# Kernel optimization log

Measured on AMD Instinct MI355X. Metric: run time of the kernel, lower is better.

The kernel has to match this reference:

```python
import jax, jax.numpy as jnp
import numpy as np

NUM_HEADS, NUM_KEYS, NUM_VALUES, NUM_OUTPUTS = 8, 64, 64, 512
B, H, W, C = 16, 64, 64, 512


def setup_inputs() -> dict:
    key = jax.random.key(0)
    ks = jax.random.split(key, 5)
    def xavier(k, shape):
        fan_in, fan_out = shape
        lim = np.sqrt(6.0 / (fan_in + fan_out))
        return jax.random.uniform(k, shape, jnp.float32, -lim, lim)
    return {
        "x": jax.random.normal(ks[0], (B, H, W, C), jnp.float32),
        "Wq": xavier(ks[1], (C, NUM_HEADS * NUM_KEYS)),
        "bq": jnp.zeros((NUM_HEADS * NUM_KEYS,), jnp.float32),
        "Wk": xavier(ks[2], (C, NUM_HEADS * NUM_KEYS)),
        "bk": jnp.zeros((NUM_HEADS * NUM_KEYS,), jnp.float32),
        "Wv": xavier(ks[3], (C, NUM_HEADS * NUM_VALUES)),
        "bv": jnp.zeros((NUM_HEADS * NUM_VALUES,), jnp.float32),
        "Wo": xavier(ks[4], (NUM_VALUES, NUM_OUTPUTS)),
        "bo": jnp.zeros((NUM_OUTPUTS,), jnp.float32),
    }


def reference(x, Wq, bq, Wk, bk, Wv, bv, Wo, bo):
    b, h, w, c = x.shape
    n, dk, dv = NUM_HEADS, NUM_KEYS, NUM_VALUES
    # single pooled query per image
    q = (jnp.mean(x, axis=(1, 2)) @ Wq + bq).reshape(b, n, dk)      # [B,N,dk]
    K = (x @ Wk + bk).reshape(b, h, w, n, dk)                        # [B,H,W,N,dk]
    V = (x @ Wv + bv).reshape(b, h, w, n, dv)                        # [B,H,W,N,dv]
    scale = 1.0 / jnp.sqrt(jnp.float32(dk))
    # scores of the single query against every pixel
    s = jnp.einsum('bnk,bhwnk->bnhw', q, K) * scale                  # [B,N,H,W]
    attn_h = jax.nn.softmax(s, axis=-1)   # per row, softmax over width
    attn_v = jax.nn.softmax(s, axis=-2)   # per column, softmax over height
    A_h = jnp.einsum('bnhw,bhwnv->bnhv', attn_h, V)                  # [B,N,H,dv]
    A_v = jnp.einsum('bnhw,bhwnv->bnwv', attn_v, V)                  # [B,N,W,dv]
    # outer-product combine over spatial dims, summed over heads
    A = jnp.einsum('bnhv,bnwv->bhwv', A_h, A_v)                      # [B,H,W,dv]
    return A @ Wo + bo                                               # [B,H,W,num_outputs]
```

## Files before the change

kernel.cpp:

```cpp
#include <hip/hip_runtime.h>
#include <hip/hip_bf16.h>

#define NHEADS 8
#define DK 64
#define DV 64
#define CIN 512
#define PIX_PER_IMG 4096
#define NPIX 65536

typedef short bf16x8 __attribute__((ext_vector_type(8)));
typedef float f32x4 __attribute__((ext_vector_type(4)));

__device__ __forceinline__ float b2f(unsigned int u) {
  union { unsigned int i; float f; } v; v.i = u << 16; return v.f;
}
__device__ __forceinline__ unsigned short f2b(float f) {
  union { float f; unsigned int i; } v; v.f = f;
  unsigned int x = v.i;
  return (unsigned short)((x + 0x7fffu + ((x >> 16) & 1u)) >> 16);
}
__device__ __forceinline__ void gload_lds16(const void* g, void* l) {
  __builtin_amdgcn_global_load_lds(
      (const __attribute__((address_space(1))) void*)g,
      (__attribute__((address_space(3))) void*)l, 16, 0, 0);
}

__global__ __launch_bounds__(256) void k_pool_prep(
    const float* __restrict__ x, unsigned short* __restrict__ xb,
    float* __restrict__ partial,
    const float* __restrict__ Wv, const float* __restrict__ Wo,
    unsigned short* __restrict__ WvT, unsigned short* __restrict__ WoT) {
  int blk = blockIdx.x;
  int t = threadIdx.x;
  if (blk >= 2048) {
    int idx = (blk - 2048) * 256 + t;
    if (idx < 262144) {
      int n = idx >> 9, c = idx & 511;
      WvT[idx] = f2b(Wv[(size_t)c * 512 + n]);
    } else {
      int j = idx - 262144;
      int o = j >> 6, kk = j & 63;
      WoT[j] = f2b(Wo[(size_t)kk * 512 + o]);
    }
    return;
  }
  __shared__ float4 sh[128];
  int b = blk >> 7, chunk = blk & 127;
  int c4 = t & 127;
  int half = t >> 7;
  size_t rowbase = (size_t)b * PIX_PER_IMG + chunk * 32;
  const float4* x4 = (const float4*)x;
  float4 acc = make_float4(0.f, 0.f, 0.f, 0.f);
#pragma unroll
  for (int i = 0; i < 16; ++i) {
    int p = 2 * i + half;
    float4 v = x4[(rowbase + p) * 128 + c4];
    acc.x += v.x; acc.y += v.y; acc.z += v.z; acc.w += v.w;
    uint2 o;
    o.x = (unsigned)f2b(v.x) | ((unsigned)f2b(v.y) << 16);
    o.y = (unsigned)f2b(v.z) | ((unsigned)f2b(v.w) << 16);
    *(uint2*)(xb + (rowbase + p) * CIN + c4 * 4) = o;
  }
  if (half) sh[c4] = acc;
  __syncthreads();
  if (!half) {
    float4 o = sh[c4];
    acc.x += o.x; acc.y += o.y; acc.z += o.z; acc.w += o.w;
    *(float4*)(partial + (size_t)blk * CIN + c4 * 4) = acc;
  }
}

__global__ __launch_bounds__(256) void k_qp2(
    const float* __restrict__ partial,
    const float* __restrict__ Wq, const float* __restrict__ bq,
    const float* __restrict__ Wk, float* __restrict__ P) {
  __shared__ float xs[CIN];
  __shared__ float red[256];
  __shared__ float qsh[64];
  int b = blockIdx.x, n = blockIdx.y, t = threadIdx.x;
  for (int c = t; c < CIN; c += 256) {
    float s = 0.f;
    for (int ch = 0; ch < 128; ++ch) s += partial[((size_t)(b * 128 + ch)) * CIN + c];
    xs[c] = s * (1.0f / 4096.0f);
  }
  __syncthreads();
  int jj = t & 63, part = t >> 6;
  {
    float acc = 0.f;
    const float* wp = Wq + (size_t)(part * 128) * CIN + n * 64 + jj;
    for (int ci = 0; ci < 128; ++ci)
      acc += xs[part * 128 + ci] * wp[(size_t)ci * CIN];
    red[t] = acc;
  }
  __syncthreads();
  if (t < 64)
    qsh[t] = red[t] + red[t + 64] + red[t + 128] + red[t + 192] + bq[n * 64 + t];
  __syncthreads();
  for (int c = t; c < CIN; c += 256) {
    float acc = 0.f;
    const float* wr = Wk + (size_t)c * CIN + n * 64;
    for (int k = 0; k < 64; ++k) acc += qsh[k] * wr[k];
    P[((size_t)(b * NHEADS + n)) * CIN + c] = acc * 0.125f;
  }
}

__global__ __launch_bounds__(256) void k_scores(
    const unsigned short* __restrict__ xb, const float* __restrict__ P,
    float* __restrict__ s) {
  __shared__ __align__(16) unsigned short Pl[24 * 520];
  int blk = blockIdx.x;
  int b = blk >> 6, tile = blk & 63;
  int t = threadIdx.x;
  for (int i = t; i < 4096; i += 256) {
    int n = i >> 9, c = i & 511;
    float pv = P[((size_t)(b * NHEADS + n)) * CIN + c];
    unsigned short h = f2b(pv);
    Pl[n * 520 + c] = h;
    Pl[(n + 8) * 520 + c] = f2b(pv - b2f(h));
  }
  __syncthreads();
  int wave = t >> 6, lane = t & 63;
  int prow = lane & 15, kgrp = lane >> 4;
  const unsigned short* arow =
      xb + ((size_t)b * PIX_PER_IMG + tile * 64 + wave * 16 + prow) * CIN + kgrp * 8;
  const unsigned short* bhi = Pl + prow * 520 + kgrp * 8;
  const unsigned short* blo = Pl + (prow + 8) * 520 + kgrp * 8;
  f32x4 acc = (f32x4){0.f, 0.f, 0.f, 0.f};
#pragma unroll
  for (int kb = 0; kb < 16; ++kb) {
    bf16x8 af = *(const bf16x8*)(arow + kb * 32);
    bf16x8 bh = *(const bf16x8*)(bhi + kb * 32);
    bf16x8 bl = *(const bf16x8*)(blo + kb * 32);
    acc = __builtin_amdgcn_mfma_f32_16x16x32_bf16(af, bh, acc, 0, 0, 0);
    acc = __builtin_amdgcn_mfma_f32_16x16x32_bf16(af, bl, acc, 0, 0, 0);
  }
  int n = prow;
  if (n < 8) {
    float* sp = s + ((size_t)(b * NHEADS + n)) * PIX_PER_IMG + tile * 64 + wave * 16 + kgrp * 4;
#pragma unroll
    for (int r = 0; r < 4; ++r) sp[r] = acc[r];
  }
}

__global__ __launch_bounds__(256) void k_xhv(
    const unsigned short* __restrict__ xb, const float* __restrict__ s,
    unsigned short* __restrict__ XHV) {
  __shared__ unsigned short xs[64 * 256];
  __shared__ float al[NHEADS * 64];
  int bx = blockIdx.x, ch = blockIdx.y, t = threadIdx.x;
  bool isV = bx >= 1024;
  int bi = isV ? bx - 1024 : bx;
  int b = bi >> 6, rc = bi & 63;
  if (!isV) {
    const unsigned short* src = xb + ((size_t)(b * PIX_PER_IMG + rc * 64)) * CIN + ch * 256;
#pragma unroll
    for (int i = 0; i < 8; ++i) {
      int idx = i * 256 + t;
      int w = idx >> 5, off = idx & 31;
      ((uint4*)xs)[idx] = ((const uint4*)(src + (size_t)w * CIN))[off];
    }
  } else {
#pragma unroll
    for (int i = 0; i < 8; ++i) {
      int idx = i * 256 + t;
      int h = idx >> 5, off = idx & 31;
      ((uint4*)xs)[idx] =
          ((const uint4*)(xb + ((size_t)(b * PIX_PER_IMG + h * 64 + rc)) * CIN + ch * 256))[off];
    }
  }
  {
    int n = t >> 5, l = t & 31;
    const float* sp = s + ((size_t)(b * NHEADS + n)) * PIX_PER_IMG;
    float v0, v1;
    if (!isV) { v0 = sp[rc * 64 + 2 * l];  v1 = sp[rc * 64 + 2 * l + 1]; }
    else      { v0 = sp[(2 * l) * 64 + rc]; v1 = sp[(2 * l + 1) * 64 + rc]; }
    float m = fmaxf(v0, v1);
#pragma unroll
    for (int mask = 1; mask <= 16; mask <<= 1) m = fmaxf(m, __shfl_xor(m, mask));
    float e0 = __expf(v0 - m), e1 = __expf(v1 - m);
    float sm = e0 + e1;
#pragma unroll
    for (int mask = 1; mask <= 16; mask <<= 1) sm += __shfl_xor(sm, mask);
    float inv = 1.f / sm;
    al[n * 64 + 2 * l] = e0 * inv;
    al[n * 64 + 2 * l + 1] = e1 * inv;
  }
  __syncthreads();
  int n = t >> 5, oct = t & 31;
  float acc[8] = {0.f, 0.f, 0.f, 0.f, 0.f, 0.f, 0.f, 0.f};
  const float* ar = al + n * 64;
  for (int p = 0; p < 64; ++p) {
    float aw = ar[p];
    uint4 u = *(const uint4*)(xs + (size_t)p * 256 + oct * 8);
    acc[0] += aw * b2f(u.x & 0xffff);
    acc[1] += aw * b2f(u.x >> 16);
    acc[2] += aw * b2f(u.y & 0xffff);
    acc[3] += aw * b2f(u.y >> 16);
    acc[4] += aw * b2f(u.z & 0xffff);
    acc[5] += aw * b2f(u.z >> 16);
    acc[6] += aw * b2f(u.w & 0xffff);
    acc[7] += aw * b2f(u.w >> 16);
  }
  uint4 o;
  o.x = (unsigned)f2b(acc[0]) | ((unsigned)f2b(acc[1]) << 16);
  o.y = (unsigned)f2b(acc[2]) | ((unsigned)f2b(acc[3]) << 16);
  o.z = (unsigned)f2b(acc[4]) | ((unsigned)f2b(acc[5]) << 16);
  o.w = (unsigned)f2b(acc[6]) | ((unsigned)f2b(acc[7]) << 16);
  size_t dst = ((size_t)(n * 2048 + (isV ? 1024 : 0) + b * 64 + rc)) * CIN + ch * 256 + oct * 8;
  *(uint4*)(XHV + dst) = o;
}

__global__ __launch_bounds__(256) void k_gemm2(
    const unsigned short* __restrict__ XHV, const unsigned short* __restrict__ WvT,
    const float* __restrict__ bv, float* __restrict__ Ah, float* __restrict__ Av) {
  __shared__ __align__(16) unsigned short As[64 * 64];
  __shared__ __align__(16) unsigned short Bs[64 * 64];
  const int t = threadIdx.x;
  const int wave = t >> 6, lane = t & 63;
  const int m0 = blockIdx.x * 64, head = blockIdx.y;
  const unsigned short* A = XHV + (size_t)head * 2048 * CIN;
  const unsigned short* BT = WvT + (size_t)head * 64 * CIN;

  f32x4 acc[4];
  for (int j = 0; j < 4; ++j) acc[j] = (f32x4){0.f, 0.f, 0.f, 0.f};

  const int lrow = wave * 8 + (lane >> 3);
  const int lcolb = (lane & 7) * 16;

  for (int kt = 0; kt < 8; ++kt) {
    __syncthreads();
#pragma unroll
    for (int j = 0; j < 2; ++j)
      gload_lds16((const char*)A + ((size_t)(m0 + j * 32 + lrow) * CIN + kt * 64) * 2 + lcolb,
                  (char*)As + (j * 32 + wave * 8) * 128);
#pragma unroll
    for (int j = 0; j < 2; ++j)
      gload_lds16((const char*)BT + ((size_t)(j * 32 + lrow) * CIN + kt * 64) * 2 + lcolb,
                  (char*)Bs + (j * 32 + wave * 8) * 128);
    __syncthreads();
#pragma unroll
    for (int ss = 0; ss < 2; ++ss) {
      bf16x8 af = *(const bf16x8*)((const char*)As + (wave * 16 + (lane & 15)) * 128 +
                                   ss * 64 + ((lane >> 4) * 16));
      bf16x8 bg[4];
#pragma unroll
      for (int j = 0; j < 4; ++j)
        bg[j] = *(const bf16x8*)((const char*)Bs + (j * 16 + (lane & 15)) * 128 +
                                 ss * 64 + ((lane >> 4) * 16));
#pragma unroll
      for (int j = 0; j < 4; ++j)
        acc[j] = __builtin_amdgcn_mfma_f32_16x16x32_bf16(af, bg[j], acc[j], 0, 0, 0);
    }
  }
#pragma unroll
  for (int j = 0; j < 4; ++j) {
    int v = j * 16 + (lane & 15);
    float bb = bv[head * 64 + v];
#pragma unroll
    for (int r = 0; r < 4; ++r) {
      int m = m0 + wave * 16 + ((lane >> 4) * 4) + r;
      float val = acc[j][r] + bb;
      if (m < 1024) {
        int b = m >> 6, h = m & 63;
        Ah[((size_t)(b * NHEADS + head)) * 4096 + h * 64 + v] = val;
      } else {
        int m2 = m - 1024;
        int b = m2 >> 6, w = m2 & 63;
        Av[((size_t)(b * NHEADS + head)) * 4096 + w * 64 + v] = val;
      }
    }
  }
}

__global__ __launch_bounds__(256) void k_outgemm(
    const float* __restrict__ Ah, const float* __restrict__ Av,
    const unsigned short* __restrict__ WoT,
    const float* __restrict__ bo, float* __restrict__ out) {
  __shared__ __align__(16) unsigned short As[128 * 64];
  __shared__ __align__(16) unsigned short Bs[128 * 64];
  const int t = threadIdx.x;
  const int wave = t >> 6, lane = t & 63;
  const int wr = wave >> 1, wc = wave & 1;
  const int m0 = blockIdx.y * 128;
  const int b = m0 >> 12, h0 = (m0 >> 6) & 63;

  const int srow = wave * 32 + (lane >> 3), scolb = (lane & 7) * 16;
  {
    int n0 = blockIdx.x * 256;
#pragma unroll
    for (int j = 0; j < 4; ++j)
      gload_lds16((const char*)WoT + ((size_t)(n0 + srow + j * 8) * 64) * 2 + scolb,
                  (char*)Bs + wave * 4096 + j * 1024);
  }
  {
    const int v = t & 63, rg = t >> 6;
    float ahv0[8], ahv1[8];
#pragma unroll
    for (int n = 0; n < 8; ++n) {
      ahv0[n] = Ah[((size_t)((b * 8 + n) * 64 + h0)) * 64 + v];
      ahv1[n] = Ah[((size_t)((b * 8 + n) * 64 + h0 + 1)) * 64 + v];
    }
#pragma unroll 2
    for (int i = 0; i < 16; ++i) {
      int w = rg * 16 + i;
      float a0 = 0.f, a1 = 0.f;
#pragma unroll
      for (int n = 0; n < 8; ++n) {
        float av = Av[((size_t)((b * 8 + n) * 64 + w)) * 64 + v];
        a0 += ahv0[n] * av;
        a1 += ahv1[n] * av;
      }
      As[w * 64 + v] = f2b(a0);
      As[(64 + w) * 64 + v] = f2b(a1);
    }
  }

  for (int nt = 0; nt < 2; ++nt) {
    const int n0 = (blockIdx.x * 2 + nt) * 128;
    if (nt) {
      __syncthreads();
#pragma unroll
      for (int j = 0; j < 4; ++j)
        gload_lds16((const char*)WoT + ((size_t)(n0 + srow + j * 8) * 64) * 2 + scolb,
                    (char*)Bs + wave * 4096 + j * 1024);
    }
    __syncthreads();

    f32x4 acc[4][4];
    for (int i = 0; i < 4; ++i)
      for (int j = 0; j < 4; ++j) acc[i][j] = (f32x4){0.f, 0.f, 0.f, 0.f};
#pragma unroll
    for (int ss = 0; ss < 2; ++ss) {
      bf16x8 af[4], bg[4];
#pragma unroll
      for (int i = 0; i < 4; ++i) {
        int mrow = wr * 64 + i * 16 + (lane & 15);
        af[i] = *(const bf16x8*)((const char*)As + mrow * 128 + ss * 64 + ((lane >> 4) * 16));
      }
#pragma unroll
      for (int j = 0; j < 4; ++j) {
        int nrow = wc * 64 + j * 16 + (lane & 15);
        bg[j] = *(const bf16x8*)((const char*)Bs + nrow * 128 + ss * 64 + ((lane >> 4) * 16));
      }
#pragma unroll
      for (int i = 0; i < 4; ++i)
#pragma unroll
        for (int j = 0; j < 4; ++j)
          acc[i][j] = __builtin_amdgcn_mfma_f32_16x16x32_bf16(af[i], bg[j], acc[i][j], 0, 0, 0);
    }
#pragma unroll
    for (int i = 0; i < 4; ++i)
#pragma unroll
      for (int j = 0; j < 4; ++j) {
        int mbase = m0 + wr * 64 + i * 16 + ((lane >> 4) * 4);
        int n = n0 + wc * 64 + j * 16 + (lane & 15);
        float bb = bo[n];
#pragma unroll
        for (int r = 0; r < 4; ++r)
          out[(size_t)(mbase + r) * 512 + n] = acc[i][j][r] + bb;
      }
  }
}

extern "C" void kernel_launch(void* const* d_in, const int* in_sizes, int n_in,
                              void* d_out, int out_size, void* d_ws, size_t ws_size,
                              hipStream_t stream) {
  (void)in_sizes; (void)n_in; (void)out_size; (void)ws_size;
  const float* x = (const float*)d_in[0];
  const float* Wq = (const float*)d_in[1];
  const float* bq = (const float*)d_in[2];
  const float* Wk = (const float*)d_in[3];
  const float* Wv = (const float*)d_in[5];
  const float* bv = (const float*)d_in[6];
  const float* Wo = (const float*)d_in[7];
  const float* bo = (const float*)d_in[8];
  float* out = (float*)d_out;

  char* ws = (char*)d_ws;
  unsigned short* xb = (unsigned short*)(ws + 0);
  float* partial = (float*)(ws + 67108864);
  float* s = (float*)(ws + 71303168);
  float* P = (float*)(ws + 73400320);
  unsigned short* XHV = (unsigned short*)(ws + 73662464);
  float* Ah = (float*)(ws + 90439680);
  float* Av = (float*)(ws + 92536832);
  unsigned short* WvT = (unsigned short*)(ws + 94633984);
  unsigned short* WoT = (unsigned short*)(ws + 95158272);

  k_pool_prep<<<3200, 256, 0, stream>>>(x, xb, partial, Wv, Wo, WvT, WoT);
  k_qp2<<<dim3(16, 8), 256, 0, stream>>>(partial, Wq, bq, Wk, P);
  k_scores<<<1024, 256, 0, stream>>>(xb, P, s);
  k_xhv<<<dim3(2048, 2), 256, 0, stream>>>(xb, s, XHV);
  k_gemm2<<<dim3(32, 8), 256, 0, stream>>>(XHV, WvT, bv, Ah, Av);
  k_outgemm<<<dim3(2, 512), 256, 0, stream>>>(Ah, Av, WoT, bo, out);
}
```

Before: 349.6 us.

## Fuse score computation into row/column softmax-weighted pooling kernel

```diff
diff --git a/kernel.cpp b/kernel.cpp
--- a/kernel.cpp
+++ b/kernel.cpp
@@ -104,76 +104,67 @@
   }
 }
 
-__global__ __launch_bounds__(256) void k_scores(
+__global__ __launch_bounds__(512) void k_xhv(
     const unsigned short* __restrict__ xb, const float* __restrict__ P,
-    float* __restrict__ s) {
-  __shared__ __align__(16) unsigned short Pl[24 * 520];
-  int blk = blockIdx.x;
-  int b = blk >> 6, tile = blk & 63;
-  int t = threadIdx.x;
-  for (int i = t; i < 4096; i += 256) {
+    unsigned short* __restrict__ XHV) {
+  __shared__ __align__(16) unsigned short Xs[64 * 512];
+  __shared__ __align__(16) char PlBuf[16 * 1024];
+  unsigned short* Pl = (unsigned short*)PlBuf;
+  float* sl = (float*)PlBuf;
+  float* al = (float*)(PlBuf + 2560);
+
+  int bx = blockIdx.x, t = threadIdx.x;
+  bool isV = bx >= 1024;
+  int bi = isV ? bx - 1024 : bx;
+  int b = bi >> 6, rc = bi & 63;
+
+  {
+    const unsigned short* base = xb + (size_t)b * PIX_PER_IMG * CIN;
+#pragma unroll
+    for (int i = 0; i < 8; ++i) {
+      int idx = i * 512 + t;
+      int p = idx >> 6, off = idx & 63;
+      int pix = isV ? (p * 64 + rc) : (rc * 64 + p);
+      uint4 u = ((const uint4*)(base + (size_t)pix * CIN))[off];
+      *(uint4*)((char*)Xs + p * 1024 + ((off * 16) ^ ((p & 7) << 4))) = u;
+    }
+  }
+  for (int i = t; i < 4096; i += 512) {
     int n = i >> 9, c = i & 511;
     float pv = P[((size_t)(b * NHEADS + n)) * CIN + c];
     unsigned short h = f2b(pv);
-    Pl[n * 520 + c] = h;
-    Pl[(n + 8) * 520 + c] = f2b(pv - b2f(h));
-  }
-  __syncthreads();
+    int sw = (n & 7) << 4;
+    *(unsigned short*)(PlBuf + n * 1024 + ((2 * c) ^ sw)) = h;
+    *(unsigned short*)(PlBuf + (n + 8) * 1024 + ((2 * c) ^ sw)) = f2b(pv - b2f(h));
+  }
+  __syncthreads();
+
   int wave = t >> 6, lane = t & 63;
   int prow = lane & 15, kgrp = lane >> 4;
-  const unsigned short* arow =
-      xb + ((size_t)b * PIX_PER_IMG + tile * 64 + wave * 16 + prow) * CIN + kgrp * 8;
-  const unsigned short* bhi = Pl + prow * 520 + kgrp * 8;
-  const unsigned short* blo = Pl + (prow + 8) * 520 + kgrp * 8;
-  f32x4 acc = (f32x4){0.f, 0.f, 0.f, 0.f};
-#pragma unroll
-  for (int kb = 0; kb < 16; ++kb) {
-    bf16x8 af = *(const bf16x8*)(arow + kb * 32);
-    bf16x8 bh = *(const bf16x8*)(bhi + kb * 32);
-    bf16x8 bl = *(const bf16x8*)(blo + kb * 32);
-    acc = __builtin_amdgcn_mfma_f32_16x16x32_bf16(af, bh, acc, 0, 0, 0);
-    acc = __builtin_amdgcn_mfma_f32_16x16x32_bf16(af, bl, acc, 0, 0, 0);
-  }
-  int n = prow;
-  if (n < 8) {
-    float* sp = s + ((size_t)(b * NHEADS + n)) * PIX_PER_IMG + tile * 64 + wave * 16 + kgrp * 4;
-#pragma unroll
-    for (int r = 0; r < 4; ++r) sp[r] = acc[r];
-  }
-}
-
-__global__ __launch_bounds__(256) void k_xhv(
-    const unsigned short* __restrict__ xb, const float* __restrict__ s,
-    unsigned short* __restrict__ XHV) {
-  __shared__ unsigned short xs[64 * 256];
-  __shared__ float al[NHEADS * 64];
-  int bx = blockIdx.x, ch = blockIdx.y, t = threadIdx.x;
-  bool isV = bx >= 1024;
-  int bi = isV ? bx - 1024 : bx;
-  int b = bi >> 6, rc = bi & 63;
-  if (!isV) {
-    const unsigned short* src = xb + ((size_t)(b * PIX_PER_IMG + rc * 64)) * CIN + ch * 256;
-#pragma unroll
-    for (int i = 0; i < 8; ++i) {
-      int idx = i * 256 + t;
-      int w = idx >> 5, off = idx & 31;
-      ((uint4*)xs)[idx] = ((const uint4*)(src + (size_t)w * CIN))[off];
-    }
-  } else {
-#pragma unroll
-    for (int i = 0; i < 8; ++i) {
-      int idx = i * 256 + t;
-      int h = idx >> 5, off = idx & 31;
-      ((uint4*)xs)[idx] =
-          ((const uint4*)(xb + ((size_t)(b * PIX_PER_IMG + h * 64 + rc)) * CIN + ch * 256))[off];
-    }
-  }
-  {
+  f32x4 sacc = (f32x4){0.f, 0.f, 0.f, 0.f};
+  if (wave < 4) {
+    int arow = wave * 16 + prow;
+    int asw = (arow & 7) << 4, bsw = (prow & 7) << 4;
+#pragma unroll
+    for (int kb = 0; kb < 16; ++kb) {
+      int co = kb * 64 + kgrp * 16;
+      bf16x8 af = *(const bf16x8*)((const char*)Xs + arow * 1024 + (co ^ asw));
+      bf16x8 bh = *(const bf16x8*)(PlBuf + prow * 1024 + (co ^ bsw));
+      bf16x8 bl = *(const bf16x8*)(PlBuf + (prow + 8) * 1024 + (co ^ bsw));
+      sacc = __builtin_amdgcn_mfma_f32_16x16x32_bf16(af, bh, sacc, 0, 0, 0);
+      sacc = __builtin_amdgcn_mfma_f32_16x16x32_bf16(af, bl, sacc, 0, 0, 0);
+    }
+  }
+  __syncthreads();
+  if (wave < 4 && prow < 8) {
+#pragma unroll
+    for (int r = 0; r < 4; ++r) sl[(wave * 16 + kgrp * 4 + r) * 9 + prow] = sacc[r];
+  }
+  __syncthreads();
+
+  if (t < 256) {
     int n = t >> 5, l = t & 31;
-    const float* sp = s + ((size_t)(b * NHEADS + n)) * PIX_PER_IMG;
-    float v0, v1;
-    if (!isV) { v0 = sp[rc * 64 + 2 * l];  v1 = sp[rc * 64 + 2 * l + 1]; }
-    else      { v0 = sp[(2 * l) * 64 + rc]; v1 = sp[(2 * l + 1) * 64 + rc]; }
+    float v0 = sl[(2 * l) * 9 + n], v1 = sl[(2 * l + 1) * 9 + n];
     float m = fmaxf(v0, v1);
 #pragma unroll
     for (int mask = 1; mask <= 16; mask <<= 1) m = fmaxf(m, __shfl_xor(m, mask));
@@ -186,28 +177,31 @@
     al[n * 64 + 2 * l + 1] = e1 * inv;
   }
   __syncthreads();
-  int n = t >> 5, oct = t & 31;
-  float acc[8] = {0.f, 0.f, 0.f, 0.f, 0.f, 0.f, 0.f, 0.f};
-  const float* ar = al + n * 64;
-  for (int p = 0; p < 64; ++p) {
-    float aw = ar[p];
-    uint4 u = *(const uint4*)(xs + (size_t)p * 256 + oct * 8);
-    acc[0] += aw * b2f(u.x & 0xffff);
-    acc[1] += aw * b2f(u.x >> 16);
-    acc[2] += aw * b2f(u.y & 0xffff);
-    acc[3] += aw * b2f(u.y >> 16);
-    acc[4] += aw * b2f(u.z & 0xffff);
-    acc[5] += aw * b2f(u.z >> 16);
-    acc[6] += aw * b2f(u.w & 0xffff);
-    acc[7] += aw * b2f(u.w >> 16);
-  }
-  uint4 o;
-  o.x = (unsigned)f2b(acc[0]) | ((unsigned)f2b(acc[1]) << 16);
-  o.y = (unsigned)f2b(acc[2]) | ((unsigned)f2b(acc[3]) << 16);
-  o.z = (unsigned)f2b(acc[4]) | ((unsigned)f2b(acc[5]) << 16);
-  o.w = (unsigned)f2b(acc[6]) | ((unsigned)f2b(acc[7]) << 16);
-  size_t dst = ((size_t)(n * 2048 + (isV ? 1024 : 0) + b * 64 + rc)) * CIN + ch * 256 + oct * 8;
-  *(uint4*)(XHV + dst) = o;
+
+  {
+    int n = wave, l = lane;
+    float acc[8] = {0.f, 0.f, 0.f, 0.f, 0.f, 0.f, 0.f, 0.f};
+    const float* ar = al + n * 64;
+    for (int p = 0; p < 64; ++p) {
+      float aw = ar[p];
+      uint4 u = *(const uint4*)((const char*)Xs + p * 1024 + ((l * 16) ^ ((p & 7) << 4)));
+      acc[0] += aw * b2f(u.x & 0xffff);
+      acc[1] += aw * b2f(u.x >> 16);
+      acc[2] += aw * b2f(u.y & 0xffff);
+      acc[3] += aw * b2f(u.y >> 16);
+      acc[4] += aw * b2f(u.z & 0xffff);
+      acc[5] += aw * b2f(u.z >> 16);
+      acc[6] += aw * b2f(u.w & 0xffff);
+      acc[7] += aw * b2f(u.w >> 16);
+    }
+    uint4 o;
+    o.x = (unsigned)f2b(acc[0]) | ((unsigned)f2b(acc[1]) << 16);
+    o.y = (unsigned)f2b(acc[2]) | ((unsigned)f2b(acc[3]) << 16);
+    o.z = (unsigned)f2b(acc[4]) | ((unsigned)f2b(acc[5]) << 16);
+    o.w = (unsigned)f2b(acc[6]) | ((unsigned)f2b(acc[7]) << 16);
+    size_t dst = ((size_t)(n * 2048 + (isV ? 1024 : 0) + b * 64 + rc)) * CIN + l * 8;
+    *(uint4*)(XHV + dst) = o;
+  }
 }
 
 __global__ __launch_bounds__(256) void k_gemm2(
@@ -379,18 +373,16 @@
   char* ws = (char*)d_ws;
   unsigned short* xb = (unsigned short*)(ws + 0);
   float* partial = (float*)(ws + 67108864);
-  float* s = (float*)(ws + 71303168);
-  float* P = (float*)(ws + 73400320);
-  unsigned short* XHV = (unsigned short*)(ws + 73662464);
-  float* Ah = (float*)(ws + 90439680);
-  float* Av = (float*)(ws + 92536832);
-  unsigned short* WvT = (unsigned short*)(ws + 94633984);
-  unsigned short* WoT = (unsigned short*)(ws + 95158272);
+  float* P = (float*)(ws + 71303168);
+  unsigned short* XHV = (unsigned short*)(ws + 71565312);
+  float* Ah = (float*)(ws + 88342528);
+  float* Av = (float*)(ws + 90439680);
+  unsigned short* WvT = (unsigned short*)(ws + 92536832);
+  unsigned short* WoT = (unsigned short*)(ws + 93061120);
 
   k_pool_prep<<<3200, 256, 0, stream>>>(x, xb, partial, Wv, Wo, WvT, WoT);
   k_qp2<<<dim3(16, 8), 256, 0, stream>>>(partial, Wq, bq, Wk, P);
-  k_scores<<<1024, 256, 0, stream>>>(xb, P, s);
-  k_xhv<<<dim3(2048, 2), 256, 0, stream>>>(xb, s, XHV);
+  k_xhv<<<2048, 512, 0, stream>>>(xb, P, XHV);
   k_gemm2<<<dim3(32, 8), 256, 0, stream>>>(XHV, WvT, bv, Ah, Av);
   k_outgemm<<<dim3(2, 512), 256, 0, stream>>>(Ah, Av, WoT, bo, out);
 }
```

Measured after the change: 356.8 us. +2.1%, slower.
